# Kernel optimization log

Measured on AMD Instinct MI355X. Metric: run time of the kernel, lower is better.

## Reference

```python
import jax, jax.numpy as jnp
import numpy as np

IN_COUNT, OUT_COUNT, NUM_BASIS = 512, 512, 8
X_MIN, X_MAX, GAMMA_SCALE = 0.0, 1.0, 3.0
BATCH = 8192


def setup_inputs() -> dict:
    key = jax.random.key(0)
    k_x, k_c = jax.random.split(key)
    x = jax.random.uniform(k_x, (BATCH, IN_COUNT), dtype=jnp.float32)
    coeffs = 0.01 * jax.random.normal(k_c, (OUT_COUNT, IN_COUNT, NUM_BASIS), dtype=jnp.float32)
    centers_1d = jnp.linspace(X_MIN, X_MAX, NUM_BASIS, dtype=jnp.float32)
    centers = jnp.tile(centers_1d[None, :], (IN_COUNT, 1))  # (in, basis)
    delta = (X_MAX - X_MIN) / (NUM_BASIS - 1)
    gamma = GAMMA_SCALE / delta
    slopes = jnp.full((IN_COUNT, NUM_BASIS), gamma, dtype=jnp.float32)
    return {"x": x, "coeffs": coeffs, "centers": centers, "slopes": slopes}


def reference(x, coeffs, centers, slopes):
    # s_im(x) = 0.5 * (1 + tanh(gamma_im * (x_bi - c_im)))  -> (batch, in, basis)
    basis = 0.5 * (1.0 + jnp.tanh(slopes[None, :, :] * (x[:, :, None] - centers[None, :, :])))
    # y_bj = sum_{i,m} a_jim * s_bim : fused double reduction (GEMM-shaped)
    y = jnp.einsum('bim,jim->bj', basis, coeffs)
    return y
```

## Files before the change

### kernel.cpp

```cpp
#include <hip/hip_runtime.h>

#define BATCH 8192
#define INC   512
#define OUTC  512
#define NB    8
#define KDIM  (INC * NB)

#define BM 64
#define BN 128
#define BK 64
#define NKT (KDIM / BK)
#define LDA 72
#define THREADS 256

typedef __attribute__((ext_vector_type(8))) short bf16x8;
typedef __attribute__((ext_vector_type(4))) float f32x4;
typedef __attribute__((ext_vector_type(4))) int   i32x4;

static __device__ __forceinline__ unsigned int pk2(float lo, float hi) {
    return __builtin_amdgcn_perm(__builtin_bit_cast(unsigned int, hi),
                                 __builtin_bit_cast(unsigned int, lo),
                                 0x07060302u);
}

__global__ __launch_bounds__(256)
void w_prepass(const float* __restrict__ W, unsigned short* __restrict__ Wb) {
    const int base = (blockIdx.x * 256 + threadIdx.x) * 8;
    const float4 a = *(const float4*)(W + base);
    const float4 b = *(const float4*)(W + base + 4);
    const float v[8] = {a.x, a.y, a.z, a.w, b.x, b.y, b.z, b.w};
    unsigned int r[8];
#pragma unroll
    for (int i = 0; i < 8; ++i) {
        unsigned int t = __builtin_bit_cast(unsigned int, v[i]);
        t += 0x7FFFu + ((t >> 16) & 1u);
        r[i] = t >> 16;
    }
    i32x4 out = {(int)(r[0] | (r[1] << 16)), (int)(r[2] | (r[3] << 16)),
                 (int)(r[4] | (r[5] << 16)), (int)(r[6] | (r[7] << 16))};
    *(i32x4*)(Wb + base) = out;
}


template <bool DMA>
__global__ __launch_bounds__(THREADS, 2)
void tanh_basis_fused_gemm(const float* __restrict__ X,
                           const void*  __restrict__ Wsrc,
                           const float* __restrict__ CEN,
                           const float* __restrict__ SLP,
                           float* __restrict__ Y)
{
    __shared__ short As[2][BM][LDA];
    __shared__ short Bs[2][BN * BK];

    const int tid  = threadIdx.x;
    const int lane = tid & 63;
    const int wave = tid >> 6;
    const int wm   = wave & 1;
    const int wn   = wave >> 1;

    const int b0 = blockIdx.x * BM;
    const int j0 = blockIdx.y * BN;

    const float L2E = 1.4426950408889634f;
    const float g2  = 2.0f * SLP[0] * L2E;
    const float pc  = -g2;
    const float q0  = g2 * CEN[0];
    const float R   = __builtin_amdgcn_exp2f(g2 * (CEN[1] - CEN[0]));

    const int arow = tid >> 2;
    const int acol = (tid & 3) * 2;
    const float* xp = X + (size_t)(b0 + arow) * INC + acol;

    f32x4 acc[2][4];
#pragma unroll
    for (int i = 0; i < 2; ++i)
#pragma unroll
        for (int j = 0; j < 4; ++j)
            acc[i][j] = (f32x4){0.f, 0.f, 0.f, 0.f};

    const int aoff = (wm * 32 + (lane & 15)) * LDA + (lane >> 4) * 8;
    const int brow = wn * 64 + (lane & 15);
    const int low3 = lane & 7;
    const int h    = lane >> 4;
    const int boff0 = brow * BK + ((h)     ^ low3) * 8;
    const int boff1 = brow * BK + ((4 + h) ^ low3) * 8;

    const int dma_r    = lane >> 3;
    const int dma_kblk = (lane & 7) ^ dma_r;

    auto stage_B = [&](int kt, short* bs) {
        if constexpr (DMA) {
            const unsigned short* Wb = (const unsigned short*)Wsrc;
#pragma unroll
            for (int q = 0; q < 4; ++q) {
                const int cc = wave * 4 + q;
                const unsigned short* gp = Wb
                    + (size_t)(j0 + cc * 8 + dma_r) * KDIM
                    + kt * BK + dma_kblk * 8;
                __builtin_amdgcn_global_load_lds(
                    (const __attribute__((address_space(1))) void*)gp,
                    (__attribute__((address_space(3))) void*)(bs + cc * 512),
                    16, 0, 0);
            }
        } else {
            const float* Wf = (const float*)Wsrc;
            const int frow = tid >> 1;
            const int fkh  = tid & 1;
            const float* wp = Wf + (size_t)(j0 + frow) * KDIM + kt * BK + fkh * 32;
            float4 cv[8];
#pragma unroll
            for (int q = 0; q < 8; ++q) cv[q] = ((const float4*)wp)[q];
#pragma unroll
            for (int kb = 0; kb < 4; ++kb) {
                const int kblk = fkh * 4 + kb;
                i32x4* bw = (i32x4*)(bs + frow * BK + ((kblk ^ (frow & 7)) * 8));
                *bw = (i32x4){(int)pk2(cv[2*kb].x, cv[2*kb].y),
                              (int)pk2(cv[2*kb].z, cv[2*kb].w),
                              (int)pk2(cv[2*kb+1].x, cv[2*kb+1].y),
                              (int)pk2(cv[2*kb+1].z, cv[2*kb+1].w)};
            }
        }
    };

    auto stage_A = [&](float2 xq, short* as_base) {
        float e = __builtin_amdgcn_exp2f(fmaf(pc, xq.x, q0));
        float s[NB];
#pragma unroll
        for (int m = 0; m < NB; ++m) {
            s[m] = __builtin_amdgcn_rcpf(1.0f + e);
            e *= R;
        }
        *(i32x4*)(as_base + arow * LDA + acol * 8) =
            (i32x4){(int)pk2(s[0], s[1]), (int)pk2(s[2], s[3]),
                    (int)pk2(s[4], s[5]), (int)pk2(s[6], s[7])};

        e = __builtin_amdgcn_exp2f(fmaf(pc, xq.y, q0));
#pragma unroll
        for (int m = 0; m < NB; ++m) {
            s[m] = __builtin_amdgcn_rcpf(1.0f + e);
            e *= R;
        }
        *(i32x4*)(as_base + arow * LDA + (acol + 1) * 8) =
            (i32x4){(int)pk2(s[0], s[1]), (int)pk2(s[2], s[3]),
                    (int)pk2(s[4], s[5]), (int)pk2(s[6], s[7])};
    };

    auto mfma_tile = [&](const short* abase, const short* bbase) {
#pragma unroll
        for (int ks = 0; ks < 2; ++ks) {
            const int boffk = ks ? boff1 : boff0;
            bf16x8 af[2], bfr[4];
#pragma unroll
            for (int mf = 0; mf < 2; ++mf)
                af[mf] = *(const bf16x8*)(abase + aoff + mf * 16 * LDA + ks * 32);
#pragma unroll
            for (int nf = 0; nf < 4; ++nf)
                bfr[nf] = *(const bf16x8*)(bbase + boffk + nf * 16 * BK);
#pragma unroll
            for (int mf = 0; mf < 2; ++mf)
#pragma unroll
                for (int nf = 0; nf < 4; ++nf)
                    acc[mf][nf] = __builtin_amdgcn_mfma_f32_16x16x32_bf16(
                        af[mf], bfr[nf], acc[mf][nf], 0, 0, 0);
        }
    };

    float2 xv = *(const float2*)(xp);
    float2 xn = *(const float2*)(xp + NB);
    stage_B(0, &Bs[0][0]);
    stage_A(xv, &As[0][0][0]);
    xv = xn;

#define STEP(KT, CUR, NXT)                                                   \
    {                                                                        \
        const int kt_ = (KT);                                                \
        const int kx_ = (kt_ + 2 < NKT) ? kt_ + 2 : NKT - 1;                 \
        const int kb_ = (kt_ + 1 < NKT) ? kt_ + 1 : NKT - 1;                 \
        xn = *(const float2*)(xp + kx_ * NB);                                \
        stage_B(kb_, &Bs[NXT][0]);                                           \
        stage_A(xv, &As[NXT][0][0]);                                         \
        __builtin_amdgcn_sched_barrier(0);                                   \
        asm volatile("s_waitcnt vmcnt(5) lgkmcnt(0)" ::: "memory");          \
        __builtin_amdgcn_s_barrier();                                        \
        __builtin_amdgcn_sched_barrier(0);                                   \
        __builtin_amdgcn_s_setprio(1);                                       \
        mfma_tile(&As[CUR][0][0], &Bs[CUR][0]);                              \
        __builtin_amdgcn_s_setprio(0);                                       \
        __builtin_amdgcn_sched_barrier(0);                                   \
        __builtin_amdgcn_s_barrier();                                        \
        __builtin_amdgcn_sched_barrier(0);                                   \
        xv = xn;                                                             \
    }

    for (int kt2 = 0; kt2 < NKT; kt2 += 2) {
        STEP(kt2,     0, 1);
        STEP(kt2 + 1, 1, 0);
    }
#undef STEP

    asm volatile("s_waitcnt vmcnt(0) lgkmcnt(0)" ::: "memory");

    const int lm = (lane >> 4) * 4;
    const int ln = lane & 15;
    const int rowb = b0 + wm * 32 + lm;
    const int colb = j0 + wn * 64 + ln;
#pragma unroll
    for (int mf = 0; mf < 2; ++mf)
#pragma unroll
        for (int nf = 0; nf < 4; ++nf)
#pragma unroll
            for (int r = 0; r < 4; ++r)
                Y[(size_t)(rowb + mf * 16 + r) * OUTC + (colb + nf * 16)] = acc[mf][nf][r];
}

extern "C" void kernel_launch(void* const* d_in, const int* in_sizes, int n_in,
                              void* d_out, int out_size, void* d_ws, size_t ws_size,
                              hipStream_t stream) {
    const float* X   = (const float*)d_in[0];
    const float* W   = (const float*)d_in[1];
    const float* CEN = (const float*)d_in[2];
    const float* SLP = (const float*)d_in[3];
    float* Y = (float*)d_out;

    static_assert(BATCH % BM == 0 && OUTC % BN == 0 && KDIM % BK == 0, "tiling");
    dim3 grid(BATCH / BM, OUTC / BN);

    const size_t WB_BYTES = (size_t)OUTC * KDIM * sizeof(unsigned short);
    if (ws_size >= WB_BYTES) {
        w_prepass<<<dim3((OUTC * KDIM) / (8 * 256)), dim3(256), 0, stream>>>(
            W, (unsigned short*)d_ws);
        tanh_basis_fused_gemm<true><<<grid, dim3(THREADS), 0, stream>>>(
            X, d_ws, CEN, SLP, Y);
    } else {
        tanh_basis_fused_gemm<false><<<grid, dim3(THREADS), 0, stream>>>(
            X, (const void*)W, CEN, SLP, Y);
    }
}
```

Measured before the change: 122.9 us.

## Compute basis fragments in registers, drop A LDS staging, add split-K with atomics

The tanh-basis A operand is now built directly in registers as MFMA fragments, so each wave computes its own rows instead of staging them through shared memory. This removes the As buffer, which lowers LDS use and permits four blocks per CU. K is split across two blocks along grid z, and partial sums are accumulated into Y with atomics. The W prepass now also zeroes Y. The trade-off is that each wave recomputes basis values redundantly across the wn waves, and atomic adds make the summation order nondeterministic.

```diff
diff --git a/kernel.cpp b/kernel.cpp
--- a/kernel.cpp
+++ b/kernel.cpp
@@ -9,8 +9,7 @@
 #define BM 64
 #define BN 128
 #define BK 64
-#define NKT (KDIM / BK)
-#define LDA 72
+#define KSPLIT 2
 #define THREADS 256
 
 typedef __attribute__((ext_vector_type(8))) short bf16x8;
@@ -24,8 +23,10 @@
 }
 
 __global__ __launch_bounds__(256)
-void w_prepass(const float* __restrict__ W, unsigned short* __restrict__ Wb) {
-    const int base = (blockIdx.x * 256 + threadIdx.x) * 8;
+void w_prepass(const float* __restrict__ W, unsigned short* __restrict__ Wb,
+               float* __restrict__ Y) {
+    const int gid  = blockIdx.x * 256 + threadIdx.x;
+    const int base = gid * 8;
     const float4 a = *(const float4*)(W + base);
     const float4 b = *(const float4*)(W + base + 4);
     const float v[8] = {a.x, a.y, a.z, a.w, b.x, b.y, b.z, b.w};
@@ -39,18 +40,22 @@
     i32x4 out = {(int)(r[0] | (r[1] << 16)), (int)(r[2] | (r[3] << 16)),
                  (int)(r[4] | (r[5] << 16)), (int)(r[6] | (r[7] << 16))};
     *(i32x4*)(Wb + base) = out;
-}
-
-
-template <bool DMA>
-__global__ __launch_bounds__(THREADS, 2)
+
+    float4* yp = (float4*)Y + (size_t)gid * 4;
+    const float4 z = {0.f, 0.f, 0.f, 0.f};
+#pragma unroll
+    for (int i = 0; i < 4; ++i) yp[i] = z;
+}
+
+
+template <bool DMA, bool SPLIT>
+__global__ __launch_bounds__(THREADS, 4)
 void tanh_basis_fused_gemm(const float* __restrict__ X,
                            const void*  __restrict__ Wsrc,
                            const float* __restrict__ CEN,
                            const float* __restrict__ SLP,
                            float* __restrict__ Y)
 {
-    __shared__ short As[2][BM][LDA];
     __shared__ short Bs[2][BN * BK];
 
     const int tid  = threadIdx.x;
@@ -61,6 +66,8 @@
 
     const int b0 = blockIdx.x * BM;
     const int j0 = blockIdx.y * BN;
+    constexpr int NKTB = SPLIT ? (KDIM / BK / KSPLIT) : (KDIM / BK);
+    const int kt0 = SPLIT ? blockIdx.z * NKTB : 0;
 
     const float L2E = 1.4426950408889634f;
     const float g2  = 2.0f * SLP[0] * L2E;
@@ -68,9 +75,10 @@
     const float q0  = g2 * CEN[0];
     const float R   = __builtin_amdgcn_exp2f(g2 * (CEN[1] - CEN[0]));
 
-    const int arow = tid >> 2;
-    const int acol = (tid & 3) * 2;
-    const float* xp = X + (size_t)(b0 + arow) * INC + acol;
+    const int rl = lane & 15;
+    const int h  = lane >> 4;
+    const float* xr0 = X + (size_t)(b0 + wm * 32 + rl) * INC + h;
+    const float* xr1 = xr0 + 16 * INC;
 
     f32x4 acc[2][4];
 #pragma unroll
@@ -79,10 +87,8 @@
         for (int j = 0; j < 4; ++j)
             acc[i][j] = (f32x4){0.f, 0.f, 0.f, 0.f};
 
-    const int aoff = (wm * 32 + (lane & 15)) * LDA + (lane >> 4) * 8;
-    const int brow = wn * 64 + (lane & 15);
+    const int brow = wn * 64 + rl;
     const int low3 = lane & 7;
-    const int h    = lane >> 4;
     const int boff0 = brow * BK + ((h)     ^ low3) * 8;
     const int boff1 = brow * BK + ((4 + h) ^ low3) * 8;
 
@@ -123,95 +129,83 @@
         }
     };
 
-    auto stage_A = [&](float2 xq, short* as_base) {
-        float e = __builtin_amdgcn_exp2f(fmaf(pc, xq.x, q0));
+    auto octet = [&](float x) -> bf16x8 {
+        float e = __builtin_amdgcn_exp2f(fmaf(pc, x, q0));
         float s[NB];
 #pragma unroll
         for (int m = 0; m < NB; ++m) {
             s[m] = __builtin_amdgcn_rcpf(1.0f + e);
             e *= R;
         }
-        *(i32x4*)(as_base + arow * LDA + acol * 8) =
-            (i32x4){(int)pk2(s[0], s[1]), (int)pk2(s[2], s[3]),
-                    (int)pk2(s[4], s[5]), (int)pk2(s[6], s[7])};
-
-        e = __builtin_amdgcn_exp2f(fmaf(pc, xq.y, q0));
-#pragma unroll
-        for (int m = 0; m < NB; ++m) {
-            s[m] = __builtin_amdgcn_rcpf(1.0f + e);
-            e *= R;
-        }
-        *(i32x4*)(as_base + arow * LDA + (acol + 1) * 8) =
-            (i32x4){(int)pk2(s[0], s[1]), (int)pk2(s[2], s[3]),
-                    (int)pk2(s[4], s[5]), (int)pk2(s[6], s[7])};
+        i32x4 r = {(int)pk2(s[0], s[1]), (int)pk2(s[2], s[3]),
+                   (int)pk2(s[4], s[5]), (int)pk2(s[6], s[7])};
+        return __builtin_bit_cast(bf16x8, r);
     };
 
-    auto mfma_tile = [&](const short* abase, const short* bbase) {
-#pragma unroll
-        for (int ks = 0; ks < 2; ++ks) {
-            const int boffk = ks ? boff1 : boff0;
-            bf16x8 af[2], bfr[4];
-#pragma unroll
-            for (int mf = 0; mf < 2; ++mf)
-                af[mf] = *(const bf16x8*)(abase + aoff + mf * 16 * LDA + ks * 32);
-#pragma unroll
-            for (int nf = 0; nf < 4; ++nf)
-                bfr[nf] = *(const bf16x8*)(bbase + boffk + nf * 16 * BK);
-#pragma unroll
-            for (int mf = 0; mf < 2; ++mf)
-#pragma unroll
-                for (int nf = 0; nf < 4; ++nf)
-                    acc[mf][nf] = __builtin_amdgcn_mfma_f32_16x16x32_bf16(
-                        af[mf], bfr[nf], acc[mf][nf], 0, 0, 0);
-        }
-    };
-
-    float2 xv = *(const float2*)(xp);
-    float2 xn = *(const float2*)(xp + NB);
-    stage_B(0, &Bs[0][0]);
-    stage_A(xv, &As[0][0][0]);
-    xv = xn;
-
-#define STEP(KT, CUR, NXT)                                                   \
+    stage_B(kt0, &Bs[0][0]);
+    float x00 = xr0[(size_t)kt0 * 8];
+    float x01 = xr0[(size_t)kt0 * 8 + 4];
+    float x10 = xr1[(size_t)kt0 * 8];
+    float x11 = xr1[(size_t)kt0 * 8 + 4];
+    float n00, n01, n10, n11;
+
+#define STEP(RT, CUR, NXT)                                                   \
     {                                                                        \
-        const int kt_ = (KT);                                                \
-        const int kx_ = (kt_ + 2 < NKT) ? kt_ + 2 : NKT - 1;                 \
-        const int kb_ = (kt_ + 1 < NKT) ? kt_ + 1 : NKT - 1;                 \
-        xn = *(const float2*)(xp + kx_ * NB);                                \
-        stage_B(kb_, &Bs[NXT][0]);                                           \
-        stage_A(xv, &As[NXT][0][0]);                                         \
+        const int rn_ = ((RT) + 1 < NKTB) ? (RT) + 1 : NKTB - 1;             \
+        stage_B(kt0 + rn_, &Bs[NXT][0]);                                     \
+        n00 = xr0[(size_t)(kt0 + rn_) * 8];                                  \
+        n01 = xr0[(size_t)(kt0 + rn_) * 8 + 4];                              \
+        n10 = xr1[(size_t)(kt0 + rn_) * 8];                                  \
+        n11 = xr1[(size_t)(kt0 + rn_) * 8 + 4];                              \
+        bf16x8 af[2][2];                                                     \
+        af[0][0] = octet(x00); af[1][0] = octet(x01);                        \
+        af[0][1] = octet(x10); af[1][1] = octet(x11);                        \
         __builtin_amdgcn_sched_barrier(0);                                   \
-        asm volatile("s_waitcnt vmcnt(5) lgkmcnt(0)" ::: "memory");          \
+        asm volatile("s_waitcnt vmcnt(8) lgkmcnt(0)" ::: "memory");          \
         __builtin_amdgcn_s_barrier();                                        \
         __builtin_amdgcn_sched_barrier(0);                                   \
+        const short* bbase = &Bs[CUR][0];                                    \
+        bf16x8 bfr[2][4];                                                    \
+        _Pragma("unroll") for (int nf = 0; nf < 4; ++nf) {                   \
+            bfr[0][nf] = *(const bf16x8*)(bbase + boff0 + nf * 16 * BK);     \
+            bfr[1][nf] = *(const bf16x8*)(bbase + boff1 + nf * 16 * BK);     \
+        }                                                                    \
         __builtin_amdgcn_s_setprio(1);                                       \
-        mfma_tile(&As[CUR][0][0], &Bs[CUR][0]);                              \
+        _Pragma("unroll") for (int ks = 0; ks < 2; ++ks)                     \
+            _Pragma("unroll") for (int mf = 0; mf < 2; ++mf)                 \
+                _Pragma("unroll") for (int nf = 0; nf < 4; ++nf)             \
+                    acc[mf][nf] = __builtin_amdgcn_mfma_f32_16x16x32_bf16(   \
+                        af[ks][mf], bfr[ks][nf], acc[mf][nf], 0, 0, 0);      \
         __builtin_amdgcn_s_setprio(0);                                       \
         __builtin_amdgcn_sched_barrier(0);                                   \
         __builtin_amdgcn_s_barrier();                                        \
-        __builtin_amdgcn_sched_barrier(0);                                   \
-        xv = xn;                                                             \
-    }
-
-    for (int kt2 = 0; kt2 < NKT; kt2 += 2) {
-        STEP(kt2,     0, 1);
-        STEP(kt2 + 1, 1, 0);
+        x00 = n00; x01 = n01; x10 = n10; x11 = n11;                          \
+    }
+
+    for (int it = 0; it < NKTB; it += 2) {
+        STEP(it,     0, 1);
+        STEP(it + 1, 1, 0);
     }
 #undef STEP
 
     asm volatile("s_waitcnt vmcnt(0) lgkmcnt(0)" ::: "memory");
 
-    const int lm = (lane >> 4) * 4;
-    const int ln = lane & 15;
+    const int lm = h * 4;
     const int rowb = b0 + wm * 32 + lm;
-    const int colb = j0 + wn * 64 + ln;
+    const int colb = j0 + wn * 64 + rl;
 #pragma unroll
     for (int mf = 0; mf < 2; ++mf)
 #pragma unroll
         for (int nf = 0; nf < 4; ++nf)
 #pragma unroll
-            for (int r = 0; r < 4; ++r)
-                Y[(size_t)(rowb + mf * 16 + r) * OUTC + (colb + nf * 16)] = acc[mf][nf][r];
+            for (int rr = 0; rr < 4; ++rr) {
+                const size_t idx = (size_t)(rowb + mf * 16 + rr) * OUTC
+                                 + (colb + nf * 16);
+                if constexpr (SPLIT)
+                    unsafeAtomicAdd(&Y[idx], acc[mf][nf][rr]);
+                else
+                    Y[idx] = acc[mf][nf][rr];
+            }
 }
 
 extern "C" void kernel_launch(void* const* d_in, const int* in_sizes, int n_in,
@@ -223,17 +217,19 @@
     const float* SLP = (const float*)d_in[3];
     float* Y = (float*)d_out;
 
-    static_assert(BATCH % BM == 0 && OUTC % BN == 0 && KDIM % BK == 0, "tiling");
-    dim3 grid(BATCH / BM, OUTC / BN);
+    static_assert(BATCH % BM == 0 && OUTC % BN == 0 && KDIM % (BK * KSPLIT) == 0,
+                  "tiling");
 
     const size_t WB_BYTES = (size_t)OUTC * KDIM * sizeof(unsigned short);
     if (ws_size >= WB_BYTES) {
         w_prepass<<<dim3((OUTC * KDIM) / (8 * 256)), dim3(256), 0, stream>>>(
-            W, (unsigned short*)d_ws);
-        tanh_basis_fused_gemm<true><<<grid, dim3(THREADS), 0, stream>>>(
+            W, (unsigned short*)d_ws, Y);
+        dim3 grid(BATCH / BM, OUTC / BN, KSPLIT);
+        tanh_basis_fused_gemm<true, true><<<grid, dim3(THREADS), 0, stream>>>(
             X, d_ws, CEN, SLP, Y);
     } else {
-        tanh_basis_fused_gemm<false><<<grid, dim3(THREADS), 0, stream>>>(
+        dim3 grid(BATCH / BM, OUTC / BN, 1);
+        tanh_basis_fused_gemm<false, false><<<grid, dim3(THREADS), 0, stream>>>(
             X, (const void*)W, CEN, SLP, Y);
     }
 }
```

Result: slower. 165.6 us (+34.8%).
